# Kernel tuning notes

Hardware: AMD Instinct MI355X
Metric: run time of the kernel (lower is better)

The kernel has to match this reference:

```python
import jax, jax.numpy as jnp
import numpy as np

N = 50000      # nodes
E = 800000     # edges (before self-loops)
IN = 128       # input_dim
HID = 64       # hidden_dim
EMB = 32       # embedding_dim
HEADS = 4
NEG_SLOPE = 0.2
BN_EPS = 1e-5


def setup_inputs() -> dict:
    key = jax.random.key(0)
    ks = jax.random.split(key, 20)
    s = 0.1
    x = jax.random.normal(ks[0], (N, IN), jnp.float32)
    edge_index = jax.random.randint(ks[1], (2, E), 0, N, dtype=jnp.int64)
    # GAT layer 0: 128 -> 64, 4 heads, concat
    W0 = jax.random.normal(ks[2], (IN, HEADS * HID), jnp.float32) * s
    a_src0 = jax.random.normal(ks[3], (HEADS, HID), jnp.float32) * s
    a_dst0 = jax.random.normal(ks[4], (HEADS, HID), jnp.float32) * s
    b0 = jax.random.normal(ks[5], (HEADS * HID,), jnp.float32) * s
    # BatchNorm1d(256) in eval mode (running stats)
    bn_gamma = jax.random.uniform(ks[6], (HEADS * HID,), jnp.float32, 0.5, 1.5)
    bn_beta = jax.random.normal(ks[7], (HEADS * HID,), jnp.float32) * s
    bn_mean = jax.random.normal(ks[8], (HEADS * HID,), jnp.float32) * s
    bn_var = jax.random.uniform(ks[9], (HEADS * HID,), jnp.float32, 0.5, 1.5)
    # GAT layer 1: 256 -> 32, 1 head, mean (concat=False)
    W1 = jax.random.normal(ks[10], (HEADS * HID, EMB), jnp.float32) * s
    a_src1 = jax.random.normal(ks[11], (1, EMB), jnp.float32) * s
    a_dst1 = jax.random.normal(ks[12], (1, EMB), jnp.float32) * s
    b1 = jax.random.normal(ks[13], (EMB,), jnp.float32) * s
    # prediction head: Linear(32,64) -> ReLU -> Linear(64,1)
    head_W1 = jax.random.normal(ks[14], (EMB, HID), jnp.float32) * s
    head_b1 = jax.random.normal(ks[15], (HID,), jnp.float32) * s
    head_W2 = jax.random.normal(ks[16], (HID, 1), jnp.float32) * s
    head_b2 = jax.random.normal(ks[17], (1,), jnp.float32) * s
    return dict(x=x, edge_index=edge_index, W0=W0, a_src0=a_src0, a_dst0=a_dst0, b0=b0,
                bn_gamma=bn_gamma, bn_beta=bn_beta, bn_mean=bn_mean, bn_var=bn_var,
                W1=W1, a_src1=a_src1, a_dst1=a_dst1, b1=b1,
                head_W1=head_W1, head_b1=head_b1, head_W2=head_W2, head_b2=head_b2)


def _gat_conv(x, src, dst, W, a_src, a_dst, bias, heads, out_c, concat):
    # PyG GATConv (eval mode, dropout off, self-loops already in src/dst)
    n = x.shape[0]
    h = (x @ W).reshape(n, heads, out_c)                # [N,H,C]
    alpha_s = jnp.sum(h * a_src, axis=-1)               # [N,H]
    alpha_d = jnp.sum(h * a_dst, axis=-1)               # [N,H]
    e = alpha_s[src] + alpha_d[dst]                      # [Etot,H]
    e = jnp.where(e > 0, e, NEG_SLOPE * e)               # leaky_relu
    m = jax.ops.segment_max(e, dst, num_segments=n)      # softmax over incoming edges
    e = jnp.exp(e - m[dst])
    denom = jax.ops.segment_sum(e, dst, num_segments=n)
    alpha = e / denom[dst]                               # [Etot,H]; self-loops ensure denom>0
    out = jax.ops.segment_sum(h[src] * alpha[:, :, None], dst, num_segments=n)  # [N,H,C]
    out = out.reshape(n, heads * out_c) if concat else out.mean(axis=1)
    return out + bias


def reference(x, edge_index, W0, a_src0, a_dst0, b0,
              bn_gamma, bn_beta, bn_mean, bn_var,
              W1, a_src1, a_dst1, b1,
              head_W1, head_b1, head_W2, head_b2):
    n = x.shape[0]
    loops = jnp.arange(n, dtype=edge_index.dtype)
    src = jnp.concatenate([edge_index[0], loops])
    dst = jnp.concatenate([edge_index[1], loops])

    h = _gat_conv(x, src, dst, W0, a_src0, a_dst0, b0, HEADS, HID, True)   # [N,256]
    h = (h - bn_mean) * (bn_gamma / jnp.sqrt(bn_var + BN_EPS)) + bn_beta   # BN eval
    h = jax.nn.relu(h)                                                      # dropout off (eval)
    node_embeddings = _gat_conv(h, src, dst, W1, a_src1, a_dst1, b1, 1, EMB, False)  # [N,32]

    graph_embedding = jnp.mean(node_embeddings, axis=0, keepdims=True)      # [1,32]
    hid = jax.nn.relu(graph_embedding @ head_W1 + head_b1)
    predictions = hid @ head_W2 + head_b2                                    # [1,1]
    return node_embeddings, predictions
```

## Files before the change

kernel.cpp:

```cpp
#include <hip/hip_runtime.h>


#define NEG_SLOPE 0.2f
#define BN_EPS 1e-5f

typedef __attribute__((ext_vector_type(8))) short bf16x8;
typedef __attribute__((ext_vector_type(4))) float f32x4;

__device__ __forceinline__ float bf2f(unsigned short u) {
  return __uint_as_float((unsigned)u << 16);
}
__device__ __forceinline__ unsigned short f2bf(float f) {
  unsigned u = __float_as_uint(f);
  u += 0x7fff + ((u >> 16) & 1);
  return (unsigned short)(u >> 16);
}
__device__ __forceinline__ float lrelu(float x) {
  return x > 0.f ? x : NEG_SLOPE * x;
}

__global__ __launch_bounds__(256) void w_swizzle_kernel(
    const float* __restrict__ W0, const float* __restrict__ W1,
    unsigned short* __restrict__ w0sw, unsigned short* __restrict__ w1sw) {
  int o = blockIdx.x * 256 + threadIdx.x;
  if (o < 32768) {
    int j = o & 7, l = (o >> 3) & 63, ks = (o >> 9) & 3,
        ci = (o >> 11) & 3, h = (o >> 13) & 3;
    int row = ks * 32 + (l >> 4) * 8 + j;
    int col = h * 64 + ci * 16 + (l & 15);
    w0sw[o] = f2bf(W0[row * 256 + col]);
  } else if (o < 40960) {
    int o2 = o - 32768;
    int j = o2 & 7, l = (o2 >> 3) & 63, ks = (o2 >> 9) & 7, ci = (o2 >> 12) & 1;
    int row = ks * 32 + (l >> 4) * 8 + j;
    int col = ci * 16 + (l & 15);
    w1sw[o2] = f2bf(W1[row * 32 + col]);
  }
}

__global__ __launch_bounds__(256) void gemm0_mfma_kernel(
    const float* __restrict__ x, const unsigned short* __restrict__ w0sw,
    const float* __restrict__ a_src0, const float* __restrict__ a_dst0,
    unsigned short* __restrict__ h0bf, float* __restrict__ as0,
    float* __restrict__ ad0, int M) {
  __shared__ unsigned short Asw[16 * 64 * 8];
  const int t = threadIdx.x;
  const int lane = t & 63;
  const int h = t >> 6;
  const int row0 = blockIdx.x * 64;

  #pragma unroll
  for (int i = 0; i < 8; ++i) {
    int q = t + 256 * i;
    int r = q >> 5, c4 = q & 31;
    int gr = row0 + r;
    float4 v = make_float4(0.f, 0.f, 0.f, 0.f);
    if (gr < M) v = *reinterpret_cast<const float4*>(&x[(size_t)gr * 128 + c4 * 4]);
    int ks = c4 >> 3;
    int lane_hi = (c4 >> 1) & 3;
    int j0 = (c4 & 1) * 4;
    int slot = (r >> 4) * 4 + ks;
    int dlane = (r & 15) + 16 * lane_hi;
    ushort4 o;
    o.x = f2bf(v.x); o.y = f2bf(v.y); o.z = f2bf(v.z); o.w = f2bf(v.w);
    *reinterpret_cast<ushort4*>(&Asw[(slot * 64 + dlane) * 8 + j0]) = o;
  }
  __syncthreads();

  f32x4 acc[4][4] = {};
  const bf16x8* wp = reinterpret_cast<const bf16x8*>(w0sw);
  #pragma unroll
  for (int ks = 0; ks < 4; ++ks) {
    bf16x8 bfrag[4];
    #pragma unroll
    for (int ci = 0; ci < 4; ++ci)
      bfrag[ci] = wp[(h * 16 + ci * 4 + ks) * 64 + lane];
    #pragma unroll
    for (int ri = 0; ri < 4; ++ri) {
      bf16x8 af = *reinterpret_cast<const bf16x8*>(&Asw[((ri * 4 + ks) * 64 + lane) * 8]);
      #pragma unroll
      for (int ci = 0; ci < 4; ++ci)
        acc[ri][ci] = __builtin_amdgcn_mfma_f32_16x16x32_bf16(af, bfrag[ci], acc[ri][ci], 0, 0, 0);
    }
  }

  float av[4], dv[4];
  #pragma unroll
  for (int ci = 0; ci < 4; ++ci) {
    av[ci] = a_src0[h * 64 + ci * 16 + (lane & 15)];
    dv[ci] = a_dst0[h * 64 + ci * 16 + (lane & 15)];
  }
  const int mrow = (lane >> 4) * 4;
  #pragma unroll
  for (int ri = 0; ri < 4; ++ri) {
    #pragma unroll
    for (int r = 0; r < 4; ++r) {
      int gr = row0 + ri * 16 + mrow + r;
      float ps = acc[ri][0][r] * av[0] + acc[ri][1][r] * av[1] +
                 acc[ri][2][r] * av[2] + acc[ri][3][r] * av[3];
      float pd = acc[ri][0][r] * dv[0] + acc[ri][1][r] * dv[1] +
                 acc[ri][2][r] * dv[2] + acc[ri][3][r] * dv[3];
      #pragma unroll
      for (int off = 1; off < 16; off <<= 1) {
        ps += __shfl_xor(ps, off);
        pd += __shfl_xor(pd, off);
      }
      if (gr < M) {
        #pragma unroll
        for (int ci = 0; ci < 4; ++ci)
          h0bf[(size_t)gr * 256 + h * 64 + ci * 16 + (lane & 15)] = f2bf(acc[ri][ci][r]);
        if ((lane & 15) == 0) { as0[gr * 4 + h] = ps; ad0[gr * 4 + h] = pd; }
      }
    }
  }
}

__global__ __launch_bounds__(256) void gemm1_mfma_kernel(
    const unsigned short* __restrict__ agg0bf,
    const unsigned short* __restrict__ w1sw,
    const float* __restrict__ a_src1, const float* __restrict__ a_dst1,
    unsigned short* __restrict__ h1bf, float* __restrict__ as1,
    float* __restrict__ ad1, int M) {
  const int t = threadIdx.x;
  const int lane = t & 63;
  const int w = t >> 6;
  const int rbase = blockIdx.x * 64 + w * 16;
  const int arow = rbase + (lane & 15);
  const int ar = arow < M ? arow : M - 1;
  const bf16x8* ap = reinterpret_cast<const bf16x8*>(agg0bf) + (size_t)ar * 32;
  const bf16x8* bp = reinterpret_cast<const bf16x8*>(w1sw);

  f32x4 acc[2] = {};
  #pragma unroll
  for (int ks = 0; ks < 8; ++ks) {
    bf16x8 af = ap[ks * 4 + (lane >> 4)];
    acc[0] = __builtin_amdgcn_mfma_f32_16x16x32_bf16(af, bp[(0 * 8 + ks) * 64 + lane], acc[0], 0, 0, 0);
    acc[1] = __builtin_amdgcn_mfma_f32_16x16x32_bf16(af, bp[(1 * 8 + ks) * 64 + lane], acc[1], 0, 0, 0);
  }

  float av[2], dv[2];
  #pragma unroll
  for (int ci = 0; ci < 2; ++ci) {
    av[ci] = a_src1[ci * 16 + (lane & 15)];
    dv[ci] = a_dst1[ci * 16 + (lane & 15)];
  }
  #pragma unroll
  for (int r = 0; r < 4; ++r) {
    int gr = rbase + (lane >> 4) * 4 + r;
    float ps = acc[0][r] * av[0] + acc[1][r] * av[1];
    float pd = acc[0][r] * dv[0] + acc[1][r] * dv[1];
    #pragma unroll
    for (int off = 1; off < 16; off <<= 1) {
      ps += __shfl_xor(ps, off);
      pd += __shfl_xor(pd, off);
    }
    if (gr < M) {
      h1bf[(size_t)gr * 32 + (lane & 15)]      = f2bf(acc[0][r]);
      h1bf[(size_t)gr * 32 + 16 + (lane & 15)] = f2bf(acc[1][r]);
      if ((lane & 15) == 0) { as1[gr] = ps; ad1[gr] = pd; }
    }
  }
}

__global__ __launch_bounds__(256) void hist_kernel(
    const int* __restrict__ dsts, int* __restrict__ deg, int E, int N) {
  int e = blockIdx.x * 256 + threadIdx.x;
  if (e >= E + N) return;
  int d = (e < E) ? dsts[e] : e - E;
  atomicAdd(&deg[d], 1);
}

__global__ __launch_bounds__(256) void scan_block_kernel(
    const int* __restrict__ deg, int* __restrict__ excl,
    int* __restrict__ bsum, int N) {
  __shared__ int tmp[256];
  int i = blockIdx.x * 256 + threadIdx.x;
  int v = (i < N) ? deg[i] : 0;
  tmp[threadIdx.x] = v;
  __syncthreads();
  #pragma unroll
  for (int off = 1; off < 256; off <<= 1) {
    int t = (threadIdx.x >= off) ? tmp[threadIdx.x - off] : 0;
    __syncthreads();
    tmp[threadIdx.x] += t;
    __syncthreads();
  }
  if (i < N) excl[i] = tmp[threadIdx.x] - v;
  if (threadIdx.x == 255) bsum[blockIdx.x] = tmp[255];
}

__global__ __launch_bounds__(256) void scan_bsum_kernel(int* __restrict__ bsum, int NB) {
  __shared__ int tmp[256];
  int i = threadIdx.x;
  int v = (i < NB) ? bsum[i] : 0;
  tmp[i] = v;
  __syncthreads();
  #pragma unroll
  for (int off = 1; off < 256; off <<= 1) {
    int t = (i >= off) ? tmp[i - off] : 0;
    __syncthreads();
    tmp[i] += t;
    __syncthreads();
  }
  if (i < NB) bsum[i] = tmp[i] - v;
}

__global__ __launch_bounds__(256) void scan_add_kernel(
    int* __restrict__ rowptr, const int* __restrict__ bsum,
    int* __restrict__ cursor, int N, int Etot) {
  int i = blockIdx.x * 256 + threadIdx.x;
  if (i < N) {
    int r = rowptr[i] + bsum[blockIdx.x];
    rowptr[i] = r;
    cursor[i] = r;
  }
  if (i == 0) rowptr[N] = Etot;
}

__global__ __launch_bounds__(256) void scatter_kernel(
    const int* __restrict__ srcs, const int* __restrict__ dsts,
    int* __restrict__ cursor, int* __restrict__ csr_src, int E, int N) {
  int e = blockIdx.x * 256 + threadIdx.x;
  if (e >= E + N) return;
  int s, d;
  if (e < E) { s = srcs[e]; d = dsts[e]; } else { s = d = e - E; }
  int pos = atomicAdd(&cursor[d], 1);
  csr_src[pos] = s;
}

__global__ __launch_bounds__(256) void agg0_kernel(
    const int* __restrict__ rowptr, const int* __restrict__ csr_src,
    const unsigned short* __restrict__ h0bf, const float* __restrict__ as0,
    const float* __restrict__ ad0, const float* __restrict__ b0,
    const float* __restrict__ gamma, const float* __restrict__ beta,
    const float* __restrict__ mean, const float* __restrict__ var,
    unsigned short* __restrict__ outbf, int N) {
  const int lane = threadIdx.x & 63;
  const int wid = threadIdx.x >> 6;
  const int n = blockIdx.x * 4 + wid;
  if (n >= N) return;
  const int h = lane >> 4;
  const int beg = rowptr[n], end = rowptr[n + 1];
  const float adv = ad0[n * 4 + h];
  float4 acc = make_float4(0.f, 0.f, 0.f, 0.f);
  float wsum = 0.f;
  int i = beg;
  for (; i + 4 <= end; i += 4) {
    int s0 = csr_src[i + 0], s1 = csr_src[i + 1],
        s2 = csr_src[i + 2], s3 = csr_src[i + 3];
    float x0 = as0[s0 * 4 + h] + adv, x1 = as0[s1 * 4 + h] + adv,
          x2 = as0[s2 * 4 + h] + adv, x3 = as0[s3 * 4 + h] + adv;
    ushort4 v0 = *reinterpret_cast<const ushort4*>(&h0bf[(size_t)s0 * 256 + lane * 4]);
    ushort4 v1 = *reinterpret_cast<const ushort4*>(&h0bf[(size_t)s1 * 256 + lane * 4]);
    ushort4 v2 = *reinterpret_cast<const ushort4*>(&h0bf[(size_t)s2 * 256 + lane * 4]);
    ushort4 v3 = *reinterpret_cast<const ushort4*>(&h0bf[(size_t)s3 * 256 + lane * 4]);
    float w0 = __expf(lrelu(x0)), w1 = __expf(lrelu(x1)),
          w2 = __expf(lrelu(x2)), w3 = __expf(lrelu(x3));
    wsum += (w0 + w1) + (w2 + w3);
    acc.x += w0 * bf2f(v0.x) + w1 * bf2f(v1.x) + w2 * bf2f(v2.x) + w3 * bf2f(v3.x);
    acc.y += w0 * bf2f(v0.y) + w1 * bf2f(v1.y) + w2 * bf2f(v2.y) + w3 * bf2f(v3.y);
    acc.z += w0 * bf2f(v0.z) + w1 * bf2f(v1.z) + w2 * bf2f(v2.z) + w3 * bf2f(v3.z);
    acc.w += w0 * bf2f(v0.w) + w1 * bf2f(v1.w) + w2 * bf2f(v2.w) + w3 * bf2f(v3.w);
  }
  for (; i < end; ++i) {
    int s = csr_src[i];
    float x = as0[s * 4 + h] + adv;
    float w = __expf(lrelu(x));
    wsum += w;
    ushort4 v = *reinterpret_cast<const ushort4*>(&h0bf[(size_t)s * 256 + lane * 4]);
    acc.x += w * bf2f(v.x); acc.y += w * bf2f(v.y);
    acc.z += w * bf2f(v.z); acc.w += w * bf2f(v.w);
  }
  float inv = 1.0f / wsum;
  int j = lane * 4;
  float4 bb = *reinterpret_cast<const float4*>(&b0[j]);
  float4 mu = *reinterpret_cast<const float4*>(&mean[j]);
  float4 gg = *reinterpret_cast<const float4*>(&gamma[j]);
  float4 vv = *reinterpret_cast<const float4*>(&var[j]);
  float4 be = *reinterpret_cast<const float4*>(&beta[j]);
  float4 o;
  o.x = (acc.x * inv + bb.x - mu.x) * (gg.x * rsqrtf(vv.x + BN_EPS)) + be.x;
  o.y = (acc.y * inv + bb.y - mu.y) * (gg.y * rsqrtf(vv.y + BN_EPS)) + be.y;
  o.z = (acc.z * inv + bb.z - mu.z) * (gg.z * rsqrtf(vv.z + BN_EPS)) + be.z;
  o.w = (acc.w * inv + bb.w - mu.w) * (gg.w * rsqrtf(vv.w + BN_EPS)) + be.w;
  ushort4 ob;
  ob.x = f2bf(fmaxf(o.x, 0.f)); ob.y = f2bf(fmaxf(o.y, 0.f));
  ob.z = f2bf(fmaxf(o.z, 0.f)); ob.w = f2bf(fmaxf(o.w, 0.f));
  *reinterpret_cast<ushort4*>(&outbf[(size_t)n * 256 + j]) = ob;
}

__global__ __launch_bounds__(256) void agg1_kernel(
    const int* __restrict__ rowptr, const int* __restrict__ csr_src,
    const unsigned short* __restrict__ h1bf, const float* __restrict__ as1,
    const float* __restrict__ ad1, const float* __restrict__ b1,
    float* __restrict__ out, int N) {
  const int t = threadIdx.x;
  const int lane = t & 63;
  const int w = t >> 6;
  const int n = blockIdx.x * 4 + w;
  if (n >= N) return;
  const int c = lane & 31;
  const int half = lane >> 5;
  const int beg = rowptr[n], end = rowptr[n + 1];
  const float adv = ad1[n];
  float acc = 0.f, wsum = 0.f;
  int i = beg + half;
  for (; i + 6 < end; i += 8) {
    int s0 = csr_src[i + 0], s1 = csr_src[i + 2],
        s2 = csr_src[i + 4], s3 = csr_src[i + 6];
    float x0 = as1[s0] + adv, x1 = as1[s1] + adv,
          x2 = as1[s2] + adv, x3 = as1[s3] + adv;
    unsigned short u0 = h1bf[(size_t)s0 * 32 + c];
    unsigned short u1 = h1bf[(size_t)s1 * 32 + c];
    unsigned short u2 = h1bf[(size_t)s2 * 32 + c];
    unsigned short u3 = h1bf[(size_t)s3 * 32 + c];
    float w0 = __expf(lrelu(x0)), w1 = __expf(lrelu(x1)),
          w2 = __expf(lrelu(x2)), w3 = __expf(lrelu(x3));
    wsum += (w0 + w1) + (w2 + w3);
    acc += w0 * bf2f(u0) + w1 * bf2f(u1) + w2 * bf2f(u2) + w3 * bf2f(u3);
  }
  for (; i < end; i += 2) {
    int s = csr_src[i];
    float wgt = __expf(lrelu(as1[s] + adv));
    wsum += wgt;
    acc += wgt * bf2f(h1bf[(size_t)s * 32 + c]);
  }
  acc += __shfl_xor(acc, 32);
  wsum += __shfl_xor(wsum, 32);
  if (half == 0) out[(size_t)n * 32 + c] = acc / wsum + b1[c];
}

__global__ __launch_bounds__(256) void gsum_kernel(
    const float* __restrict__ out, float* __restrict__ gsum, int N) {
  __shared__ float red[8][32];
  const int t = threadIdx.x;
  const int c = t & 31;
  float s = 0.f;
  const size_t total = (size_t)N * 32;
  for (size_t j = (size_t)blockIdx.x * 256 + t; j < total;
       j += (size_t)gridDim.x * 256)
    s += out[j];
  red[t >> 5][c] = s;
  __syncthreads();
  if (t < 32) {
    float v = 0.f;
    #pragma unroll
    for (int i = 0; i < 8; ++i) v += red[i][t];
    atomicAdd(&gsum[t], v);
  }
}

__global__ void pred_kernel(
    const float* __restrict__ gsum, const float* __restrict__ hW1,
    const float* __restrict__ hb1, const float* __restrict__ hW2,
    const float* __restrict__ hb2, float* __restrict__ out, int N) {
  int j = threadIdx.x;
  float invN = 1.0f / (float)N;
  float acc = hb1[j];
  #pragma unroll
  for (int c = 0; c < 32; ++c) acc += (gsum[c] * invN) * hW1[c * 64 + j];
  acc = fmaxf(acc, 0.f);
  float v = acc * hW2[j];
  #pragma unroll
  for (int off = 1; off < 64; off <<= 1) v += __shfl_xor(v, off);
  if (j == 0) out[(size_t)N * 32] = v + hb2[0];
}

extern "C" void kernel_launch(void* const* d_in, const int* in_sizes, int n_in,
                              void* d_out, int out_size, void* d_ws, size_t ws_size,
                              hipStream_t stream) {
  const float* x       = (const float*)d_in[0];
  const int*   ei      = (const int*)d_in[1];
  const float* W0      = (const float*)d_in[2];
  const float* a_src0  = (const float*)d_in[3];
  const float* a_dst0  = (const float*)d_in[4];
  const float* b0      = (const float*)d_in[5];
  const float* bn_g    = (const float*)d_in[6];
  const float* bn_b    = (const float*)d_in[7];
  const float* bn_m    = (const float*)d_in[8];
  const float* bn_v    = (const float*)d_in[9];
  const float* W1      = (const float*)d_in[10];
  const float* a_src1  = (const float*)d_in[11];
  const float* a_dst1  = (const float*)d_in[12];
  const float* b1      = (const float*)d_in[13];
  const float* hW1     = (const float*)d_in[14];
  const float* hb1     = (const float*)d_in[15];
  const float* hW2     = (const float*)d_in[16];
  const float* hb2     = (const float*)d_in[17];

  const int N = in_sizes[0] / 128;
  const int E = in_sizes[1] / 2;
  const int Etot = E + N;
  const int* srcs = ei;
  const int* dsts = ei + E;
  const int NB = (N + 255) / 256;

  float* out = (float*)d_out;

  float* ws = (float*)d_ws;
  size_t off = 0;
  unsigned short* h0bf   = (unsigned short*)(ws + off); off += (size_t)N * 128;
  unsigned short* agg0bf = (unsigned short*)(ws + off); off += (size_t)N * 128;
  unsigned short* h1bf   = (unsigned short*)(ws + off); off += (size_t)N * 16;
  unsigned short* w0sw   = (unsigned short*)(ws + off); off += 16384;
  unsigned short* w1sw   = (unsigned short*)(ws + off); off += 4096;
  float* as0    = ws + off; off += (size_t)N * 4;
  float* ad0    = ws + off; off += (size_t)N * 4;
  float* as1    = ws + off; off += (size_t)N;
  float* ad1    = ws + off; off += (size_t)N;
  int* rowptr   = (int*)(ws + off); off += (size_t)N + 1;
  int* cursor   = (int*)(ws + off); off += (size_t)N;
  int* bsum     = (int*)(ws + off); off += 256;
  int* csr_src  = (int*)(ws + off); off += (size_t)Etot;
  size_t zoff = off;
  int* deg      = (int*)(ws + off); off += (size_t)N;
  float* gsum   = ws + off; off += 32;

  hipMemsetAsync(ws + zoff, 0, (off - zoff) * sizeof(float), stream);

  auto cdiv = [](long a, long b) { return (int)((a + b - 1) / b); };

  hist_kernel<<<cdiv(Etot, 256), 256, 0, stream>>>(dsts, deg, E, N);
  scan_block_kernel<<<NB, 256, 0, stream>>>(deg, rowptr, bsum, N);
  scan_bsum_kernel<<<1, 256, 0, stream>>>(bsum, NB);
  scan_add_kernel<<<NB, 256, 0, stream>>>(rowptr, bsum, cursor, N, Etot);
  scatter_kernel<<<cdiv(Etot, 256), 256, 0, stream>>>(srcs, dsts, cursor, csr_src, E, N);

  w_swizzle_kernel<<<160, 256, 0, stream>>>(W0, W1, w0sw, w1sw);

  gemm0_mfma_kernel<<<cdiv(N, 64), 256, 0, stream>>>(
      x, w0sw, a_src0, a_dst0, h0bf, as0, ad0, N);
  agg0_kernel<<<cdiv(N, 4), 256, 0, stream>>>(rowptr, csr_src, h0bf, as0, ad0,
                                              b0, bn_g, bn_b, bn_m, bn_v, agg0bf, N);

  gemm1_mfma_kernel<<<cdiv(N, 64), 256, 0, stream>>>(
      agg0bf, w1sw, a_src1, a_dst1, h1bf, as1, ad1, N);
  agg1_kernel<<<cdiv(N, 4), 256, 0, stream>>>(rowptr, csr_src, h1bf, as1, ad1,
                                              b1, out, N);

  gsum_kernel<<<128, 256, 0, stream>>>(out, gsum, N);
  pred_kernel<<<1, 64, 0, stream>>>(gsum, hW1, hb1, hW2, hb2, out, N);
}
```

Baseline: 252.2 us.

## Cooperative edge-weight compute in agg0, exp2 scaling, fuse scan and prediction kernels

After: 258.8 us. +2.6%, slower.

```diff
diff --git a/kernel.cpp b/kernel.cpp
--- a/kernel.cpp
+++ b/kernel.cpp
@@ -3,6 +3,7 @@
 
 #define NEG_SLOPE 0.2f
 #define BN_EPS 1e-5f
+#define LOG2E 1.4426950408889634f
 
 typedef __attribute__((ext_vector_type(8))) short bf16x8;
 typedef __attribute__((ext_vector_type(4))) float f32x4;
@@ -14,9 +15,6 @@
   unsigned u = __float_as_uint(f);
   u += 0x7fff + ((u >> 16) & 1);
   return (unsigned short)(u >> 16);
-}
-__device__ __forceinline__ float lrelu(float x) {
-  return x > 0.f ? x : NEG_SLOPE * x;
 }
 
 __global__ __launch_bounds__(256) void w_swizzle_kernel(
@@ -109,7 +107,7 @@
         #pragma unroll
         for (int ci = 0; ci < 4; ++ci)
           h0bf[(size_t)gr * 256 + h * 64 + ci * 16 + (lane & 15)] = f2bf(acc[ri][ci][r]);
-        if ((lane & 15) == 0) { as0[gr * 4 + h] = ps; ad0[gr * 4 + h] = pd; }
+        if ((lane & 15) == 0) { as0[gr * 4 + h] = ps * LOG2E; ad0[gr * 4 + h] = pd * LOG2E; }
       }
     }
   }
@@ -157,7 +155,7 @@
     if (gr < M) {
       h1bf[(size_t)gr * 32 + (lane & 15)]      = f2bf(acc[0][r]);
       h1bf[(size_t)gr * 32 + 16 + (lane & 15)] = f2bf(acc[1][r]);
-      if ((lane & 15) == 0) { as1[gr] = ps; ad1[gr] = pd; }
+      if ((lane & 15) == 0) { as1[gr] = ps * LOG2E; ad1[gr] = pd * LOG2E; }
     }
   }
 }
@@ -189,28 +187,20 @@
   if (threadIdx.x == 255) bsum[blockIdx.x] = tmp[255];
 }
 
-__global__ __launch_bounds__(256) void scan_bsum_kernel(int* __restrict__ bsum, int NB) {
-  __shared__ int tmp[256];
-  int i = threadIdx.x;
-  int v = (i < NB) ? bsum[i] : 0;
-  tmp[i] = v;
-  __syncthreads();
-  #pragma unroll
-  for (int off = 1; off < 256; off <<= 1) {
-    int t = (i >= off) ? tmp[i - off] : 0;
-    __syncthreads();
-    tmp[i] += t;
-    __syncthreads();
-  }
-  if (i < NB) bsum[i] = tmp[i] - v;
-}
-
 __global__ __launch_bounds__(256) void scan_add_kernel(
     int* __restrict__ rowptr, const int* __restrict__ bsum,
     int* __restrict__ cursor, int N, int Etot) {
-  int i = blockIdx.x * 256 + threadIdx.x;
+  __shared__ int wred[4];
+  const int t = threadIdx.x;
+  int v = (t < blockIdx.x) ? bsum[t] : 0;
+  #pragma unroll
+  for (int off = 32; off >= 1; off >>= 1) v += __shfl_xor(v, off);
+  if ((t & 63) == 0) wred[t >> 6] = v;
+  __syncthreads();
+  const int prefix = wred[0] + wred[1] + wred[2] + wred[3];
+  int i = blockIdx.x * 256 + t;
   if (i < N) {
-    int r = rowptr[i] + bsum[blockIdx.x];
+    int r = rowptr[i] + prefix;
     rowptr[i] = r;
     cursor[i] = r;
   }
@@ -235,54 +225,88 @@
     const float* __restrict__ gamma, const float* __restrict__ beta,
     const float* __restrict__ mean, const float* __restrict__ var,
     unsigned short* __restrict__ outbf, int N) {
+  __shared__ float wlds[4][64];
   const int lane = threadIdx.x & 63;
   const int wid = threadIdx.x >> 6;
   const int n = blockIdx.x * 4 + wid;
   if (n >= N) return;
   const int h = lane >> 4;
+  const int eidx = lane & 15;
+  const int bb = lane & 48;
   const int beg = rowptr[n], end = rowptr[n + 1];
   const float adv = ad0[n * 4 + h];
   float4 acc = make_float4(0.f, 0.f, 0.f, 0.f);
   float wsum = 0.f;
-  int i = beg;
-  for (; i + 4 <= end; i += 4) {
-    int s0 = csr_src[i + 0], s1 = csr_src[i + 1],
-        s2 = csr_src[i + 2], s3 = csr_src[i + 3];
-    float x0 = as0[s0 * 4 + h] + adv, x1 = as0[s1 * 4 + h] + adv,
-          x2 = as0[s2 * 4 + h] + adv, x3 = as0[s3 * 4 + h] + adv;
-    ushort4 v0 = *reinterpret_cast<const ushort4*>(&h0bf[(size_t)s0 * 256 + lane * 4]);
-    ushort4 v1 = *reinterpret_cast<const ushort4*>(&h0bf[(size_t)s1 * 256 + lane * 4]);
-    ushort4 v2 = *reinterpret_cast<const ushort4*>(&h0bf[(size_t)s2 * 256 + lane * 4]);
-    ushort4 v3 = *reinterpret_cast<const ushort4*>(&h0bf[(size_t)s3 * 256 + lane * 4]);
-    float w0 = __expf(lrelu(x0)), w1 = __expf(lrelu(x1)),
-          w2 = __expf(lrelu(x2)), w3 = __expf(lrelu(x3));
-    wsum += (w0 + w1) + (w2 + w3);
-    acc.x += w0 * bf2f(v0.x) + w1 * bf2f(v1.x) + w2 * bf2f(v2.x) + w3 * bf2f(v3.x);
-    acc.y += w0 * bf2f(v0.y) + w1 * bf2f(v1.y) + w2 * bf2f(v2.y) + w3 * bf2f(v3.y);
-    acc.z += w0 * bf2f(v0.z) + w1 * bf2f(v1.z) + w2 * bf2f(v2.z) + w3 * bf2f(v3.z);
-    acc.w += w0 * bf2f(v0.w) + w1 * bf2f(v1.w) + w2 * bf2f(v2.w) + w3 * bf2f(v3.w);
-  }
-  for (; i < end; ++i) {
-    int s = csr_src[i];
-    float x = as0[s * 4 + h] + adv;
-    float w = __expf(lrelu(x));
-    wsum += w;
-    ushort4 v = *reinterpret_cast<const ushort4*>(&h0bf[(size_t)s * 256 + lane * 4]);
-    acc.x += w * bf2f(v.x); acc.y += w * bf2f(v.y);
-    acc.z += w * bf2f(v.z); acc.w += w * bf2f(v.w);
-  }
+
+  for (int i = beg; i < end; i += 16) {
+    const int rem = end - i;
+    const int ne = rem < 16 ? rem : 16;
+    const int li = (eidx < ne) ? eidx : (ne - 1);
+    const int src = csr_src[i + li];
+    float xx = as0[(unsigned)(src * 4 + h)] + adv;
+    xx = fmaxf(xx, NEG_SLOPE * xx);
+    float wl = (eidx < ne) ? exp2f(xx) : 0.f;
+    wsum += wl;
+    wlds[wid][lane] = wl;
+    int e = 0;
+    for (; e + 8 <= ne; e += 8) {
+      const int s0 = __builtin_amdgcn_readlane(src, e + 0);
+      const int s1 = __builtin_amdgcn_readlane(src, e + 1);
+      const int s2 = __builtin_amdgcn_readlane(src, e + 2);
+      const int s3 = __builtin_amdgcn_readlane(src, e + 3);
+      const int s4 = __builtin_amdgcn_readlane(src, e + 4);
+      const int s5 = __builtin_amdgcn_readlane(src, e + 5);
+      const int s6 = __builtin_amdgcn_readlane(src, e + 6);
+      const int s7 = __builtin_amdgcn_readlane(src, e + 7);
+      ushort4 v0 = *reinterpret_cast<const ushort4*>(&(h0bf + (size_t)s0 * 256)[lane * 4]);
+      ushort4 v1 = *reinterpret_cast<const ushort4*>(&(h0bf + (size_t)s1 * 256)[lane * 4]);
+      ushort4 v2 = *reinterpret_cast<const ushort4*>(&(h0bf + (size_t)s2 * 256)[lane * 4]);
+      ushort4 v3 = *reinterpret_cast<const ushort4*>(&(h0bf + (size_t)s3 * 256)[lane * 4]);
+      ushort4 v4 = *reinterpret_cast<const ushort4*>(&(h0bf + (size_t)s4 * 256)[lane * 4]);
+      ushort4 v5 = *reinterpret_cast<const ushort4*>(&(h0bf + (size_t)s5 * 256)[lane * 4]);
+      ushort4 v6 = *reinterpret_cast<const ushort4*>(&(h0bf + (size_t)s6 * 256)[lane * 4]);
+      ushort4 v7 = *reinterpret_cast<const ushort4*>(&(h0bf + (size_t)s7 * 256)[lane * 4]);
+      const float w0 = wlds[wid][bb + e + 0];
+      const float w1 = wlds[wid][bb + e + 1];
+      const float w2 = wlds[wid][bb + e + 2];
+      const float w3 = wlds[wid][bb + e + 3];
+      const float w4 = wlds[wid][bb + e + 4];
+      const float w5 = wlds[wid][bb + e + 5];
+      const float w6 = wlds[wid][bb + e + 6];
+      const float w7 = wlds[wid][bb + e + 7];
+      acc.x += ((w0 * bf2f(v0.x) + w1 * bf2f(v1.x)) + (w2 * bf2f(v2.x) + w3 * bf2f(v3.x))) +
+               ((w4 * bf2f(v4.x) + w5 * bf2f(v5.x)) + (w6 * bf2f(v6.x) + w7 * bf2f(v7.x)));
+      acc.y += ((w0 * bf2f(v0.y) + w1 * bf2f(v1.y)) + (w2 * bf2f(v2.y) + w3 * bf2f(v3.y))) +
+               ((w4 * bf2f(v4.y) + w5 * bf2f(v5.y)) + (w6 * bf2f(v6.y) + w7 * bf2f(v7.y)));
+      acc.z += ((w0 * bf2f(v0.z) + w1 * bf2f(v1.z)) + (w2 * bf2f(v2.z) + w3 * bf2f(v3.z))) +
+               ((w4 * bf2f(v4.z) + w5 * bf2f(v5.z)) + (w6 * bf2f(v6.z) + w7 * bf2f(v7.z)));
+      acc.w += ((w0 * bf2f(v0.w) + w1 * bf2f(v1.w)) + (w2 * bf2f(v2.w) + w3 * bf2f(v3.w))) +
+               ((w4 * bf2f(v4.w) + w5 * bf2f(v5.w)) + (w6 * bf2f(v6.w) + w7 * bf2f(v7.w)));
+    }
+    for (; e < ne; ++e) {
+      const int s0 = __builtin_amdgcn_readlane(src, e);
+      const float w0 = wlds[wid][bb + e];
+      ushort4 v = *reinterpret_cast<const ushort4*>(&(h0bf + (size_t)s0 * 256)[lane * 4]);
+      acc.x += w0 * bf2f(v.x); acc.y += w0 * bf2f(v.y);
+      acc.z += w0 * bf2f(v.z); acc.w += w0 * bf2f(v.w);
+    }
+  }
+
+  #pragma unroll
+  for (int off = 1; off < 16; off <<= 1) wsum += __shfl_xor(wsum, off);
+
   float inv = 1.0f / wsum;
   int j = lane * 4;
-  float4 bb = *reinterpret_cast<const float4*>(&b0[j]);
+  float4 bbv = *reinterpret_cast<const float4*>(&b0[j]);
   float4 mu = *reinterpret_cast<const float4*>(&mean[j]);
   float4 gg = *reinterpret_cast<const float4*>(&gamma[j]);
   float4 vv = *reinterpret_cast<const float4*>(&var[j]);
   float4 be = *reinterpret_cast<const float4*>(&beta[j]);
   float4 o;
-  o.x = (acc.x * inv + bb.x - mu.x) * (gg.x * rsqrtf(vv.x + BN_EPS)) + be.x;
-  o.y = (acc.y * inv + bb.y - mu.y) * (gg.y * rsqrtf(vv.y + BN_EPS)) + be.y;
-  o.z = (acc.z * inv + bb.z - mu.z) * (gg.z * rsqrtf(vv.z + BN_EPS)) + be.z;
-  o.w = (acc.w * inv + bb.w - mu.w) * (gg.w * rsqrtf(vv.w + BN_EPS)) + be.w;
+  o.x = (acc.x * inv + bbv.x - mu.x) * (gg.x * rsqrtf(vv.x + BN_EPS)) + be.x;
+  o.y = (acc.y * inv + bbv.y - mu.y) * (gg.y * rsqrtf(vv.y + BN_EPS)) + be.y;
+  o.z = (acc.z * inv + bbv.z - mu.z) * (gg.z * rsqrtf(vv.z + BN_EPS)) + be.z;
+  o.w = (acc.w * inv + bbv.w - mu.w) * (gg.w * rsqrtf(vv.w + BN_EPS)) + be.w;
   ushort4 ob;
   ob.x = f2bf(fmaxf(o.x, 0.f)); ob.y = f2bf(fmaxf(o.y, 0.f));
   ob.z = f2bf(fmaxf(o.z, 0.f)); ob.w = f2bf(fmaxf(o.w, 0.f));
@@ -314,14 +338,17 @@
     unsigned short u1 = h1bf[(size_t)s1 * 32 + c];
     unsigned short u2 = h1bf[(size_t)s2 * 32 + c];
     unsigned short u3 = h1bf[(size_t)s3 * 32 + c];
-    float w0 = __expf(lrelu(x0)), w1 = __expf(lrelu(x1)),
-          w2 = __expf(lrelu(x2)), w3 = __expf(lrelu(x3));
+    float w0 = exp2f(fmaxf(x0, NEG_SLOPE * x0)),
+          w1 = exp2f(fmaxf(x1, NEG_SLOPE * x1)),
+          w2 = exp2f(fmaxf(x2, NEG_SLOPE * x2)),
+          w3 = exp2f(fmaxf(x3, NEG_SLOPE * x3));
     wsum += (w0 + w1) + (w2 + w3);
     acc += w0 * bf2f(u0) + w1 * bf2f(u1) + w2 * bf2f(u2) + w3 * bf2f(u3);
   }
   for (; i < end; i += 2) {
     int s = csr_src[i];
-    float wgt = __expf(lrelu(as1[s] + adv));
+    float xx = as1[s] + adv;
+    float wgt = exp2f(fmaxf(xx, NEG_SLOPE * xx));
     wsum += wgt;
     acc += wgt * bf2f(h1bf[(size_t)s * 32 + c]);
   }
@@ -331,8 +358,13 @@
 }
 
 __global__ __launch_bounds__(256) void gsum_kernel(
-    const float* __restrict__ out, float* __restrict__ gsum, int N) {
+    const float* __restrict__ out, float* __restrict__ gsum,
+    int* __restrict__ ticket,
+    const float* __restrict__ hW1, const float* __restrict__ hb1,
+    const float* __restrict__ hW2, const float* __restrict__ hb2,
+    float* __restrict__ pout, int N) {
   __shared__ float red[8][32];
+  __shared__ int lastblk;
   const int t = threadIdx.x;
   const int c = t & 31;
   float s = 0.f;
@@ -348,22 +380,28 @@
     for (int i = 0; i < 8; ++i) v += red[i][t];
     atomicAdd(&gsum[t], v);
   }
-}
-
-__global__ void pred_kernel(
-    const float* __restrict__ gsum, const float* __restrict__ hW1,
-    const float* __restrict__ hb1, const float* __restrict__ hW2,
-    const float* __restrict__ hb2, float* __restrict__ out, int N) {
-  int j = threadIdx.x;
-  float invN = 1.0f / (float)N;
-  float acc = hb1[j];
-  #pragma unroll
-  for (int c = 0; c < 32; ++c) acc += (gsum[c] * invN) * hW1[c * 64 + j];
-  acc = fmaxf(acc, 0.f);
-  float v = acc * hW2[j];
-  #pragma unroll
-  for (int off = 1; off < 64; off <<= 1) v += __shfl_xor(v, off);
-  if (j == 0) out[(size_t)N * 32] = v + hb2[0];
+  __threadfence();
+  if (t == 0) {
+    int old = __hip_atomic_fetch_add(ticket, 1, __ATOMIC_ACQ_REL,
+                                     __HIP_MEMORY_SCOPE_AGENT);
+    lastblk = (old == (int)gridDim.x - 1);
+  }
+  __syncthreads();
+  if (lastblk && t < 64) {
+    float invN = 1.0f / (float)N;
+    float acc = hb1[t];
+    #pragma unroll
+    for (int cc = 0; cc < 32; ++cc) {
+      float gv = __hip_atomic_load(&gsum[cc], __ATOMIC_RELAXED,
+                                   __HIP_MEMORY_SCOPE_AGENT);
+      acc += (gv * invN) * hW1[cc * 64 + t];
+    }
+    acc = fmaxf(acc, 0.f);
+    float v = acc * hW2[t];
+    #pragma unroll
+    for (int off = 1; off < 64; off <<= 1) v += __shfl_xor(v, off);
+    if (t == 0) pout[(size_t)N * 32] = v + hb2[0];
+  }
 }
 
 extern "C" void kernel_launch(void* const* d_in, const int* in_sizes, int n_in,
@@ -415,6 +453,7 @@
   size_t zoff = off;
   int* deg      = (int*)(ws + off); off += (size_t)N;
   float* gsum   = ws + off; off += 32;
+  int* ticket   = (int*)(ws + off); off += 1;
 
   hipMemsetAsync(ws + zoff, 0, (off - zoff) * sizeof(float), stream);
 
@@ -422,7 +461,6 @@
 
   hist_kernel<<<cdiv(Etot, 256), 256, 0, stream>>>(dsts, deg, E, N);
   scan_block_kernel<<<NB, 256, 0, stream>>>(deg, rowptr, bsum, N);
-  scan_bsum_kernel<<<1, 256, 0, stream>>>(bsum, NB);
   scan_add_kernel<<<NB, 256, 0, stream>>>(rowptr, bsum, cursor, N, Etot);
   scatter_kernel<<<cdiv(Etot, 256), 256, 0, stream>>>(srcs, dsts, cursor, csr_src, E, N);
 
@@ -438,6 +476,5 @@
   agg1_kernel<<<cdiv(N, 4), 256, 0, stream>>>(rowptr, csr_src, h1bf, as1, ad1,
                                               b1, out, N);
 
-  gsum_kernel<<<128, 256, 0, stream>>>(out, gsum, N);
-  pred_kernel<<<1, 64, 0, stream>>>(gsum, hW1, hb1, hW2, hb2, out, N);
-}
+  gsum_kernel<<<128, 256, 0, stream>>>(out, gsum, ticket, hW1, hb1, hW2, hb2, out, N);
+}
```
